# Kernel optimization log

Measured on AMD Instinct MI355X. Metric: run time of the kernel, lower is better.

The kernel has to match this reference:

```python
import jax, jax.numpy as jnp
import numpy as np

BETA = 0.25  # commitment loss weight (module default beta=0.25)
K = 1024     # num_of_embeddings


def setup_inputs() -> dict:
    key = jax.random.key(0)
    k1, k2 = jax.random.split(key)
    inputs = jax.random.normal(k1, (16, 256, 64, 64), dtype=jnp.float32)  # NCHW
    codebook = jax.random.normal(k2, (K, 256), dtype=jnp.float32)         # [K, D]
    return {"inputs": inputs, "codebook": codebook}


def reference(inputs, codebook):
    # NCHW -> NHWC, flatten to [N, D]
    x = jnp.transpose(inputs, (0, 2, 3, 1))
    shape_nhwc = x.shape
    flat = x.reshape(-1, codebook.shape[1])  # [N, D]

    dist = (jnp.sum(flat * flat, axis=1, keepdims=True)
            + jnp.sum(codebook * codebook, axis=1)
            - 2.0 * flat @ codebook.T)  # [N, K]
    idx = jnp.argmin(dist, axis=1)  # [N]

    # one-hot @ codebook is just a gather
    zq = codebook[idx].reshape(shape_nhwc)  # [B, H, W, D]

    commitment_loss = jnp.mean((zq - x) ** 2)
    loss = BETA * commitment_loss

    # straight-through estimator
    zq_st = x + jax.lax.stop_gradient(zq - x)

    # perplexity: avg one-hot probs == normalized histogram of code usage
    n = flat.shape[0]
    counts = jnp.zeros((K,), dtype=flat.dtype).at[idx].add(1.0)
    avg_probs = counts / n
    perplexity = jnp.exp(-jnp.sum(avg_probs * jnp.log(avg_probs + 1e-10)))

    z_out = jnp.transpose(zq_st, (0, 3, 1, 2))  # back to NCHW
    return z_out, loss, perplexity, idx[:, None]
```

## Files before the change

### kernel.cpp

```cpp
#include <hip/hip_runtime.h>
#include <math.h>

#define NPTS   65536
#define DDIM   256
#define KCODES 1024
#define HWSZ   4096
#define ZELEMS 16777216
#define CHW    1048576


typedef __attribute__((ext_vector_type(8))) short s16x8;
typedef __attribute__((ext_vector_type(4))) float f32x4;

#define AS1 __attribute__((address_space(1)))
#define AS3 __attribute__((address_space(3)))

__device__ __forceinline__ void bf16split(float x, unsigned short& h, unsigned short& l) {
    unsigned u  = __float_as_uint(x);
    unsigned hu = (u + 0x8000u) & 0xFFFF0000u;
    h = (unsigned short)(hu >> 16);
    float r = x - __uint_as_float(hu);
    l = (unsigned short)((__float_as_uint(r) + 0x8000u) >> 16);
}

__global__ __launch_bounds__(256) void conv_w(const float* __restrict__ cb,
                                              unsigned short* __restrict__ Ws,
                                              float* __restrict__ ww) {
    int gid  = blockIdx.x * 256 + threadIdx.x;
    int code = gid >> 3, o32 = gid & 7;
    int ct = code >> 8, r256 = code & 255, rh = r256 >> 7, rr = r256 & 127;
    unsigned short hi[32], lo[32];
    float ss = 0.f;
#pragma unroll
    for (int j4 = 0; j4 < 8; ++j4) {
        float4 v = *(const float4*)(cb + (size_t)code * DDIM + o32 * 32 + j4 * 4);
        ss += v.x * v.x + v.y * v.y + v.z * v.z + v.w * v.w;
        bf16split(v.x, hi[j4*4+0], lo[j4*4+0]);
        bf16split(v.y, hi[j4*4+1], lo[j4*4+1]);
        bf16split(v.z, hi[j4*4+2], lo[j4*4+2]);
        bf16split(v.w, hi[j4*4+3], lo[j4*4+3]);
    }
    ss += __shfl_down(ss, 4, 8);
    ss += __shfl_down(ss, 2, 8);
    ss += __shfl_down(ss, 1, 8);
    if (o32 == 0) ww[code] = ss;
    size_t bh = (size_t)ct * 131072 + (size_t)o32       * 8192 + rh * 4096 + (rr >> 4) * 512;
    size_t bl = (size_t)ct * 131072 + (size_t)(o32 + 8) * 8192 + rh * 4096 + (rr >> 4) * 512;
#pragma unroll
    for (int oct = 0; oct < 4; ++oct) {
        size_t fo = (size_t)((rr & 15) + 16 * oct) * 8;
        *(s16x8*)(Ws + bh + fo) = *(const s16x8*)&hi[oct * 8];
        *(s16x8*)(Ws + bl + fo) = *(const s16x8*)&lo[oct * 8];
    }
}

__global__ __launch_bounds__(256) void conv_x(const float* __restrict__ in,
                                              unsigned short* __restrict__ Xs,
                                              float* __restrict__ xxpart) {
    __shared__ float xt[32 * 128];
    __shared__ float xps[4];
    const int tid = threadIdx.x;
    const int rg = blockIdx.x >> 3, dc = blockIdx.x & 7;
    const int mt = rg >> 1, rhalf = rg & 1;
    const int b = (rg * 128) >> 12, hw0 = (rg * 128) & 4095;
    const float* src = in + (size_t)b * CHW + (size_t)(dc * 32) * HWSZ + hw0;
    float xs = 0.f;
#pragma unroll
    for (int r = 0; r < 16; ++r) {
        int e = r * 256 + tid, dd = e >> 7, i = e & 127;
        float v = src[(size_t)dd * HWSZ + i];
        xt[dd * 128 + i] = v;
        xs += v * v;
    }
#pragma unroll
    for (int o = 32; o; o >>= 1) xs += __shfl_down(xs, o, 64);
    if ((tid & 63) == 0) xps[tid >> 6] = xs;
    __syncthreads();
    if (tid == 0) xxpart[blockIdx.x] = xps[0] + xps[1] + xps[2] + xps[3];
#pragma unroll
    for (int hl = 0; hl < 2; ++hl) {
        int g = hl * 256 + tid;
        int row = g >> 2, o = g & 3;
        unsigned short hi[8], lo[8];
#pragma unroll
        for (int j = 0; j < 8; ++j)
            bf16split(xt[(o * 8 + j) * 128 + row], hi[j], lo[j]);
        size_t fo = rhalf * 4096 + (size_t)(row >> 4) * 512 + (size_t)((row & 15) + 16 * o) * 8;
        size_t bh = (size_t)mt * 131072 + (size_t)dc       * 8192 + fo;
        size_t bl = (size_t)mt * 131072 + (size_t)(dc + 8) * 8192 + fo;
        *(s16x8*)(Xs + bh) = *(const s16x8*)hi;
        *(s16x8*)(Xs + bl) = *(const s16x8*)lo;
    }
}

__global__ __launch_bounds__(512) void gemm_argmin(
        const unsigned short* __restrict__ Xs, const unsigned short* __restrict__ Ws,
        const float* __restrict__ ww, unsigned long long* __restrict__ pbest) {
    __shared__ unsigned short lds[49152];
    const int tid = threadIdx.x, lane = tid & 63, w = tid >> 6;
    const int wm = w >> 2, wn = w & 3;
    const int col = lane & 15, q = lane >> 4;
    const int bid = blockIdx.x;
    const int xcd = bid & 7, slot = bid >> 3;
    const int nt = slot & 3, mb = (slot >> 2) * 8 + xcd;

    const unsigned short* XsB = Xs + (size_t)mb * 131072;
    const unsigned short* WsB = Ws + (size_t)nt * 131072
                              + (wn >> 1) * 4096 + (wn & 1) * 2048 + lane * 8;

    f32x4 acc[8][4] = {};
    s16x8 B0[4], B1[4];
    const int aoff = wm * 4096 + lane * 8;

    auto SA = [&](int g, int p) {
        const int kA = (g & 7) | ((g >> 4) << 3);
        const unsigned short* s0 = XsB + kA * 8192 + tid * 8;
        __builtin_amdgcn_global_load_lds((const AS1 unsigned*)s0,
            (AS3 unsigned*)&lds[p * 8192 + w * 512], 16, 0, 0);
        __builtin_amdgcn_global_load_lds((const AS1 unsigned*)(s0 + 4096),
            (AS3 unsigned*)&lds[p * 8192 + 4096 + w * 512], 16, 0, 0);
    };
    auto LB = [&](int g, s16x8* B) {
        const int kW = (g & 7) | (((g >> 3) & 1) << 3);
        const s16x8* src = (const s16x8*)(WsB + kW * 8192);
        B[0] = src[0]; B[1] = src[64]; B[2] = src[128]; B[3] = src[192];
    };
#define BAR do { __builtin_amdgcn_s_barrier(); __builtin_amdgcn_sched_barrier(0); } while (0)

    auto TILE = [&](int g, int p, int pstg, const s16x8* Bc, s16x8* Bn,
                    int gate, bool dobar) {
        s16x8 a[8];
#pragma unroll
        for (int mf = 0; mf < 8; ++mf)
            a[mf] = *(const s16x8*)&lds[p * 8192 + aoff + mf * 512];
        if (g + 1 < 24) LB(g + 1, Bn);
        if (g + 4 < 24) SA(g + 4, pstg);
        if (gate == 6)      asm volatile("s_waitcnt vmcnt(6)" ::: "memory");
        else if (gate == 4) asm volatile("s_waitcnt vmcnt(4)" ::: "memory");
        else                asm volatile("s_waitcnt vmcnt(0)" ::: "memory");
        __builtin_amdgcn_sched_barrier(0);
        __builtin_amdgcn_s_setprio(1);
#pragma unroll
        for (int mf = 0; mf < 8; ++mf) {
            acc[mf][0] = __builtin_amdgcn_mfma_f32_16x16x32_bf16(a[mf], Bc[0], acc[mf][0], 0, 0, 0);
            acc[mf][1] = __builtin_amdgcn_mfma_f32_16x16x32_bf16(a[mf], Bc[1], acc[mf][1], 0, 0, 0);
            acc[mf][2] = __builtin_amdgcn_mfma_f32_16x16x32_bf16(a[mf], Bc[2], acc[mf][2], 0, 0, 0);
            acc[mf][3] = __builtin_amdgcn_mfma_f32_16x16x32_bf16(a[mf], Bc[3], acc[mf][3], 0, 0, 0);
        }
        __builtin_amdgcn_s_setprio(0);
        if (dobar) BAR;
    };

    SA(0, 0); SA(1, 1); SA(2, 2); SA(3, 3);
    LB(0, B0);
    asm volatile("s_waitcnt vmcnt(4)" ::: "memory");
    BAR;

    for (int t6 = 0; t6 < 3; ++t6) {
        TILE(t6 * 6 + 0, 0, 4, B0, B1, 6, false);
        TILE(t6 * 6 + 1, 1, 5, B1, B0, 6, true);
        TILE(t6 * 6 + 2, 2, 0, B0, B1, 6, false);
        TILE(t6 * 6 + 3, 3, 1, B1, B0, 6, true);
        TILE(t6 * 6 + 4, 4, 2, B0, B1, 6, false);
        TILE(t6 * 6 + 5, 5, 3, B1, B0, 6, true);
    }
    TILE(18, 0, 4, B0, B1, 6, false);
    TILE(19, 1, 5, B1, B0, 6, true);
    TILE(20, 2, 0, B0, B1, 4, false);
    TILE(21, 3, 1, B1, B0, 4, true);
    TILE(22, 4, 2, B0, B1, 4, false);
    TILE(23, 5, 3, B1, B0, 0, false);

    __syncthreads();
    unsigned long long* kbuf = (unsigned long long*)lds;
    float wv[4];
#pragma unroll
    for (int nf = 0; nf < 4; ++nf) wv[nf] = ww[nt * 256 + wn * 64 + nf * 16 + col];
#pragma unroll
    for (int mf = 0; mf < 8; ++mf)
#pragma unroll
        for (int r = 0; r < 4; ++r) {
            unsigned long long key = ~0ull;
#pragma unroll
            for (int nf = 0; nf < 4; ++nf) {
                int kg = nt * 256 + wn * 64 + nf * 16 + col;
                float sd = wv[nf] - 2.f * acc[mf][nf][r];
                unsigned u = __float_as_uint(sd);
                u = (u & 0x80000000u) ? ~u : (u | 0x80000000u);
                unsigned long long kk = ((unsigned long long)u << 32) | (unsigned)kg;
                key = kk < key ? kk : key;
            }
#pragma unroll
            for (int off = 1; off < 4; off <<= 1) {
                unsigned klo = __shfl_xor((unsigned)key, off, 64);
                unsigned khi = __shfl_xor((unsigned)(key >> 32), off, 64);
                unsigned long long ok = ((unsigned long long)khi << 32) | klo;
                key = ok < key ? ok : key;
            }
            if ((col & 3) == 0)
                kbuf[(wm * 128 + mf * 16 + q * 4 + r) * 17 + wn * 4 + (col >> 2)] = key;
        }
    __syncthreads();
    if (tid < 256) {
        const unsigned long long* rowp = kbuf + tid * 17;
        unsigned long long km = rowp[0];
#pragma unroll
        for (int i = 1; i < 16; ++i) {
            unsigned long long k = rowp[i];
            km = k < km ? k : km;
        }
        pbest[(size_t)nt * 65536 + mb * 256 + tid] = km;
    }
#undef BAR
}

__global__ __launch_bounds__(256) void gather_kernel(
        const float* __restrict__ cb, const unsigned long long* __restrict__ pbest,
        float* __restrict__ idx_out, unsigned int* __restrict__ counts,
        float* __restrict__ zout, float* __restrict__ partials) {
    const int tid = threadIdx.x;
    const int n   = blockIdx.x * 256 + tid;
    unsigned long long km = pbest[n];
#pragma unroll
    for (int nt = 1; nt < 4; ++nt) {
        unsigned long long k = pbest[(size_t)nt * 65536 + n];
        km = k < km ? k : km;
    }
    const int r = (int)(km & 0xFFFFFFFFu);
    idx_out[n] = (float)r;
    atomicAdd(&counts[r], 1u);

    unsigned m = (unsigned)(km >> 32);
    m = (m & 0x80000000u) ? (m & 0x7FFFFFFFu) : ~m;
    float sd = __uint_as_float(m);

    const int b = n >> 12, hw = n & 4095;
    const float4* row4 = (const float4*)(cb + (size_t)r * DDIM);
    float* zp = zout + (size_t)b * CHW + hw;
#pragma unroll 8
    for (int c4 = 0; c4 < 64; ++c4) {
        float4 v = row4[c4];
        zp[(size_t)(c4 * 4 + 0) * HWSZ] = v.x;
        zp[(size_t)(c4 * 4 + 1) * HWSZ] = v.y;
        zp[(size_t)(c4 * 4 + 2) * HWSZ] = v.z;
        zp[(size_t)(c4 * 4 + 3) * HWSZ] = v.w;
    }
#pragma unroll
    for (int o = 32; o; o >>= 1) sd += __shfl_down(sd, o, 64);
    __shared__ float ps[4];
    if ((tid & 63) == 0) ps[tid >> 6] = sd;
    __syncthreads();
    if (tid == 0) partials[blockIdx.x] = ps[0] + ps[1] + ps[2] + ps[3];
}

__global__ __launch_bounds__(256) void final_kernel(
        const float* __restrict__ partials, const float* __restrict__ xxpart,
        const unsigned int* __restrict__ counts,
        float* __restrict__ out_loss, float* __restrict__ out_perp) {
    const int tid = threadIdx.x;
    float s = partials[tid];
#pragma unroll
    for (int i = 0; i < 16; ++i) s += xxpart[tid * 16 + i];
    float e = 0.f;
#pragma unroll
    for (int qq = 0; qq < 4; ++qq) {
        float p = (float)counts[tid * 4 + qq] * (1.f / 65536.f);
        e += p * logf(p + 1e-10f);
    }
#pragma unroll
    for (int o = 32; o; o >>= 1) {
        s += __shfl_down(s, o, 64);
        e += __shfl_down(e, o, 64);
    }
    __shared__ float ss[4], es[4];
    if ((tid & 63) == 0) { ss[tid >> 6] = s; es[tid >> 6] = e; }
    __syncthreads();
    if (tid == 0) {
        float S = ss[0] + ss[1] + ss[2] + ss[3];
        float E = es[0] + es[1] + es[2] + es[3];
        *out_loss = 0.25f * (S / (float)ZELEMS);
        *out_perp = expf(-E);
    }
}

extern "C" void kernel_launch(void* const* d_in, const int* in_sizes, int n_in,
                              void* d_out, int out_size, void* d_ws, size_t ws_size,
                              hipStream_t stream) {
    (void)in_sizes; (void)n_in; (void)out_size; (void)ws_size;
    const float* in = (const float*)d_in[0];
    const float* cb = (const float*)d_in[1];
    float* out  = (float*)d_out;
    float* zout = out;
    float* loss = out + ZELEMS;
    float* perp = out + ZELEMS + 1;
    float* idxf = out + ZELEMS + 2;

    unsigned int*       counts   = (unsigned int*)d_ws;
    float*              ww       = (float*)((char*)d_ws + 4096);
    float*              partials = (float*)((char*)d_ws + 8192);
    unsigned short*     Ws       = (unsigned short*)((char*)d_ws + 16384);
    unsigned long long* pbest    = (unsigned long long*)((char*)d_ws + 1064960);
    float*              xxpart   = (float*)((char*)d_ws + 3162112);
    unsigned short*     Xs       = (unsigned short*)zout;

    hipMemsetAsync(counts, 0, 4096, stream);
    conv_w      <<<32,   256, 0, stream>>>(cb, Ws, ww);
    conv_x      <<<4096, 256, 0, stream>>>(in, Xs, xxpart);
    gemm_argmin <<<1024, 512, 0, stream>>>(Xs, Ws, ww, pbest);
    gather_kernel<<<256, 256, 0, stream>>>(cb, pbest, idxf, counts, zout, partials);
    final_kernel <<<1,   256, 0, stream>>>(partials, xxpart, counts, loss, perp);
}
```

Measured before the change: 188.7 us.

## Load GEMM A fragments directly from global into registers, dropping LDS staging

The GEMM-argmin kernel no longer stages X tiles through shared memory with global_load_lds and a 4-deep ring of barriers and vmcnt gates. Each wave now loads its A and B fragments straight from global memory into registers, double-buffered two steps ahead. This removes barriers and LDS traffic. In exchange, A data that was shared across the four wn waves is now fetched redundantly from global/L2, register pressure rises, and latency hiding depends on the compiler's scheduling.

Result: slower. 529.7 us (+180.7%).

```diff
diff --git a/kernel.cpp b/kernel.cpp
--- a/kernel.cpp
+++ b/kernel.cpp
@@ -11,9 +11,6 @@
 
 typedef __attribute__((ext_vector_type(8))) short s16x8;
 typedef __attribute__((ext_vector_type(4))) float f32x4;
-
-#define AS1 __attribute__((address_space(1)))
-#define AS3 __attribute__((address_space(3)))
 
 __device__ __forceinline__ void bf16split(float x, unsigned short& h, unsigned short& l) {
     unsigned u  = __float_as_uint(x);
@@ -96,7 +93,7 @@
 __global__ __launch_bounds__(512) void gemm_argmin(
         const unsigned short* __restrict__ Xs, const unsigned short* __restrict__ Ws,
         const float* __restrict__ ww, unsigned long long* __restrict__ pbest) {
-    __shared__ unsigned short lds[49152];
+    __shared__ unsigned long long kbuf[256 * 17];
     const int tid = threadIdx.x, lane = tid & 63, w = tid >> 6;
     const int wm = w >> 2, wn = w & 3;
     const int col = lane & 15, q = lane >> 4;
@@ -104,75 +101,44 @@
     const int xcd = bid & 7, slot = bid >> 3;
     const int nt = slot & 3, mb = (slot >> 2) * 8 + xcd;
 
-    const unsigned short* XsB = Xs + (size_t)mb * 131072;
-    const unsigned short* WsB = Ws + (size_t)nt * 131072
-                              + (wn >> 1) * 4096 + (wn & 1) * 2048 + lane * 8;
+    const unsigned short* Aw = Xs + (size_t)mb * 131072 + wm * 4096 + lane * 8;
+    const unsigned short* Bw = Ws + (size_t)nt * 131072
+                             + (wn >> 1) * 4096 + (wn & 1) * 2048 + lane * 8;
 
     f32x4 acc[8][4] = {};
-    s16x8 B0[4], B1[4];
-    const int aoff = wm * 4096 + lane * 8;
-
-    auto SA = [&](int g, int p) {
+    s16x8 A0[8], A1[8], B0[4], B1[4];
+
+    auto LA = [&](int g, s16x8* A) {
         const int kA = (g & 7) | ((g >> 4) << 3);
-        const unsigned short* s0 = XsB + kA * 8192 + tid * 8;
-        __builtin_amdgcn_global_load_lds((const AS1 unsigned*)s0,
-            (AS3 unsigned*)&lds[p * 8192 + w * 512], 16, 0, 0);
-        __builtin_amdgcn_global_load_lds((const AS1 unsigned*)(s0 + 4096),
-            (AS3 unsigned*)&lds[p * 8192 + 4096 + w * 512], 16, 0, 0);
+        const unsigned short* src = Aw + kA * 8192;
+#pragma unroll
+        for (int mf = 0; mf < 8; ++mf) A[mf] = *(const s16x8*)(src + mf * 512);
     };
     auto LB = [&](int g, s16x8* B) {
         const int kW = (g & 7) | (((g >> 3) & 1) << 3);
-        const s16x8* src = (const s16x8*)(WsB + kW * 8192);
-        B[0] = src[0]; B[1] = src[64]; B[2] = src[128]; B[3] = src[192];
+        const unsigned short* src = Bw + kW * 8192;
+#pragma unroll
+        for (int nf = 0; nf < 4; ++nf) B[nf] = *(const s16x8*)(src + nf * 512);
     };
-#define BAR do { __builtin_amdgcn_s_barrier(); __builtin_amdgcn_sched_barrier(0); } while (0)
-
-    auto TILE = [&](int g, int p, int pstg, const s16x8* Bc, s16x8* Bn,
-                    int gate, bool dobar) {
-        s16x8 a[8];
-#pragma unroll
-        for (int mf = 0; mf < 8; ++mf)
-            a[mf] = *(const s16x8*)&lds[p * 8192 + aoff + mf * 512];
-        if (g + 1 < 24) LB(g + 1, Bn);
-        if (g + 4 < 24) SA(g + 4, pstg);
-        if (gate == 6)      asm volatile("s_waitcnt vmcnt(6)" ::: "memory");
-        else if (gate == 4) asm volatile("s_waitcnt vmcnt(4)" ::: "memory");
-        else                asm volatile("s_waitcnt vmcnt(0)" ::: "memory");
-        __builtin_amdgcn_sched_barrier(0);
-        __builtin_amdgcn_s_setprio(1);
+    auto STEP = [&](int g, s16x8* Ac, s16x8* Bc) {
 #pragma unroll
         for (int mf = 0; mf < 8; ++mf) {
-            acc[mf][0] = __builtin_amdgcn_mfma_f32_16x16x32_bf16(a[mf], Bc[0], acc[mf][0], 0, 0, 0);
-            acc[mf][1] = __builtin_amdgcn_mfma_f32_16x16x32_bf16(a[mf], Bc[1], acc[mf][1], 0, 0, 0);
-            acc[mf][2] = __builtin_amdgcn_mfma_f32_16x16x32_bf16(a[mf], Bc[2], acc[mf][2], 0, 0, 0);
-            acc[mf][3] = __builtin_amdgcn_mfma_f32_16x16x32_bf16(a[mf], Bc[3], acc[mf][3], 0, 0, 0);
+            acc[mf][0] = __builtin_amdgcn_mfma_f32_16x16x32_bf16(Ac[mf], Bc[0], acc[mf][0], 0, 0, 0);
+            acc[mf][1] = __builtin_amdgcn_mfma_f32_16x16x32_bf16(Ac[mf], Bc[1], acc[mf][1], 0, 0, 0);
+            acc[mf][2] = __builtin_amdgcn_mfma_f32_16x16x32_bf16(Ac[mf], Bc[2], acc[mf][2], 0, 0, 0);
+            acc[mf][3] = __builtin_amdgcn_mfma_f32_16x16x32_bf16(Ac[mf], Bc[3], acc[mf][3], 0, 0, 0);
         }
-        __builtin_amdgcn_s_setprio(0);
-        if (dobar) BAR;
+        if (g + 2 < 24) { LA(g + 2, Ac); LB(g + 2, Bc); }
     };
 
-    SA(0, 0); SA(1, 1); SA(2, 2); SA(3, 3);
-    LB(0, B0);
-    asm volatile("s_waitcnt vmcnt(4)" ::: "memory");
-    BAR;
-
-    for (int t6 = 0; t6 < 3; ++t6) {
-        TILE(t6 * 6 + 0, 0, 4, B0, B1, 6, false);
-        TILE(t6 * 6 + 1, 1, 5, B1, B0, 6, true);
-        TILE(t6 * 6 + 2, 2, 0, B0, B1, 6, false);
-        TILE(t6 * 6 + 3, 3, 1, B1, B0, 6, true);
-        TILE(t6 * 6 + 4, 4, 2, B0, B1, 6, false);
-        TILE(t6 * 6 + 5, 5, 3, B1, B0, 6, true);
-    }
-    TILE(18, 0, 4, B0, B1, 6, false);
-    TILE(19, 1, 5, B1, B0, 6, true);
-    TILE(20, 2, 0, B0, B1, 4, false);
-    TILE(21, 3, 1, B1, B0, 4, true);
-    TILE(22, 4, 2, B0, B1, 4, false);
-    TILE(23, 5, 3, B1, B0, 0, false);
-
-    __syncthreads();
-    unsigned long long* kbuf = (unsigned long long*)lds;
+    LA(0, A0); LB(0, B0);
+    LA(1, A1); LB(1, B1);
+#pragma unroll
+    for (int gg = 0; gg < 12; ++gg) {
+        STEP(2 * gg,     A0, B0);
+        STEP(2 * gg + 1, A1, B1);
+    }
+
     float wv[4];
 #pragma unroll
     for (int nf = 0; nf < 4; ++nf) wv[nf] = ww[nt * 256 + wn * 64 + nf * 16 + col];
@@ -211,7 +177,6 @@
         }
         pbest[(size_t)nt * 65536 + mb * 256 + tid] = km;
     }
-#undef BAR
 }
 
 __global__ __launch_bounds__(256) void gather_kernel(
```

## Halve GEMM M-tile to 128 rows, double grid, raise occupancy

Applied to the files above, without the earlier changes.

The fused distance-GEMM/argmin kernel now covers 128 rows per block instead of 256. Accumulators shrink to 4x4, LDS drops to 48 KB, and the grid doubles to 2048 blocks with launch_bounds(512,4). The vmcnt wait also moves from before the MFMAs to just before the barrier. The aim is more resident waves to hide latency, at the cost of loading the W fragments from global twice as often per output row. The looser wait placement may race with the LDS staging.

After: 179.4 us. 4.9% less time.

```diff
diff --git a/kernel.cpp b/kernel.cpp
--- a/kernel.cpp
+++ b/kernel.cpp
@@ -93,62 +93,59 @@
     }
 }
 
-__global__ __launch_bounds__(512) void gemm_argmin(
+__global__ __launch_bounds__(512, 4) void gemm_argmin(
         const unsigned short* __restrict__ Xs, const unsigned short* __restrict__ Ws,
         const float* __restrict__ ww, unsigned long long* __restrict__ pbest) {
-    __shared__ unsigned short lds[49152];
+    __shared__ unsigned short lds[24576];
     const int tid = threadIdx.x, lane = tid & 63, w = tid >> 6;
     const int wm = w >> 2, wn = w & 3;
     const int col = lane & 15, q = lane >> 4;
     const int bid = blockIdx.x;
     const int xcd = bid & 7, slot = bid >> 3;
-    const int nt = slot & 3, mb = (slot >> 2) * 8 + xcd;
-
-    const unsigned short* XsB = Xs + (size_t)mb * 131072;
-    const unsigned short* WsB = Ws + (size_t)nt * 131072
+    const int nt = slot & 3, mbi = (slot >> 2) * 8 + xcd;
+    const int mt = mbi >> 1, rh = mbi & 1;
+
+    const unsigned short* XsB = Xs + (size_t)mt * 131072 + rh * 4096;
+    const unsigned short* Bw  = Ws + (size_t)nt * 131072
                               + (wn >> 1) * 4096 + (wn & 1) * 2048 + lane * 8;
 
-    f32x4 acc[8][4] = {};
+    f32x4 acc[4][4] = {};
     s16x8 B0[4], B1[4];
-    const int aoff = wm * 4096 + lane * 8;
+    const int aoff = wm * 2048 + lane * 8;
 
     auto SA = [&](int g, int p) {
         const int kA = (g & 7) | ((g >> 4) << 3);
-        const unsigned short* s0 = XsB + kA * 8192 + tid * 8;
-        __builtin_amdgcn_global_load_lds((const AS1 unsigned*)s0,
-            (AS3 unsigned*)&lds[p * 8192 + w * 512], 16, 0, 0);
-        __builtin_amdgcn_global_load_lds((const AS1 unsigned*)(s0 + 4096),
-            (AS3 unsigned*)&lds[p * 8192 + 4096 + w * 512], 16, 0, 0);
+        __builtin_amdgcn_global_load_lds(
+            (const AS1 unsigned*)(XsB + kA * 8192 + tid * 8),
+            (AS3 unsigned*)&lds[p * 4096 + (tid >> 6) * 512 + (tid & 63) * 8], 16, 0, 0);
     };
     auto LB = [&](int g, s16x8* B) {
         const int kW = (g & 7) | (((g >> 3) & 1) << 3);
-        const s16x8* src = (const s16x8*)(WsB + kW * 8192);
+        const s16x8* src = (const s16x8*)(Bw + kW * 8192);
         B[0] = src[0]; B[1] = src[64]; B[2] = src[128]; B[3] = src[192];
     };
 #define BAR do { __builtin_amdgcn_s_barrier(); __builtin_amdgcn_sched_barrier(0); } while (0)
 
-    auto TILE = [&](int g, int p, int pstg, const s16x8* Bc, s16x8* Bn,
-                    int gate, bool dobar) {
-        s16x8 a[8];
-#pragma unroll
-        for (int mf = 0; mf < 8; ++mf)
-            a[mf] = *(const s16x8*)&lds[p * 8192 + aoff + mf * 512];
+    auto TILE = [&](int g, int p, int pstg, const s16x8* Bc, s16x8* Bn, bool sync) {
+        s16x8 a[4];
+#pragma unroll
+        for (int mf = 0; mf < 4; ++mf)
+            a[mf] = *(const s16x8*)&lds[p * 4096 + aoff + mf * 512];
         if (g + 1 < 24) LB(g + 1, Bn);
         if (g + 4 < 24) SA(g + 4, pstg);
-        if (gate == 6)      asm volatile("s_waitcnt vmcnt(6)" ::: "memory");
-        else if (gate == 4) asm volatile("s_waitcnt vmcnt(4)" ::: "memory");
-        else                asm volatile("s_waitcnt vmcnt(0)" ::: "memory");
-        __builtin_amdgcn_sched_barrier(0);
         __builtin_amdgcn_s_setprio(1);
 #pragma unroll
-        for (int mf = 0; mf < 8; ++mf) {
+        for (int mf = 0; mf < 4; ++mf) {
             acc[mf][0] = __builtin_amdgcn_mfma_f32_16x16x32_bf16(a[mf], Bc[0], acc[mf][0], 0, 0, 0);
             acc[mf][1] = __builtin_amdgcn_mfma_f32_16x16x32_bf16(a[mf], Bc[1], acc[mf][1], 0, 0, 0);
             acc[mf][2] = __builtin_amdgcn_mfma_f32_16x16x32_bf16(a[mf], Bc[2], acc[mf][2], 0, 0, 0);
             acc[mf][3] = __builtin_amdgcn_mfma_f32_16x16x32_bf16(a[mf], Bc[3], acc[mf][3], 0, 0, 0);
         }
         __builtin_amdgcn_s_setprio(0);
-        if (dobar) BAR;
+        if (sync) {
+            asm volatile("s_waitcnt vmcnt(5)" ::: "memory");
+            BAR;
+        }
     };
 
     SA(0, 0); SA(1, 1); SA(2, 2); SA(3, 3);
@@ -157,19 +154,19 @@
     BAR;
 
     for (int t6 = 0; t6 < 3; ++t6) {
-        TILE(t6 * 6 + 0, 0, 4, B0, B1, 6, false);
-        TILE(t6 * 6 + 1, 1, 5, B1, B0, 6, true);
-        TILE(t6 * 6 + 2, 2, 0, B0, B1, 6, false);
-        TILE(t6 * 6 + 3, 3, 1, B1, B0, 6, true);
-        TILE(t6 * 6 + 4, 4, 2, B0, B1, 6, false);
-        TILE(t6 * 6 + 5, 5, 3, B1, B0, 6, true);
-    }
-    TILE(18, 0, 4, B0, B1, 6, false);
-    TILE(19, 1, 5, B1, B0, 6, true);
-    TILE(20, 2, 0, B0, B1, 4, false);
-    TILE(21, 3, 1, B1, B0, 4, true);
-    TILE(22, 4, 2, B0, B1, 4, false);
-    TILE(23, 5, 3, B1, B0, 0, false);
+        TILE(t6 * 6 + 0, 0, 4, B0, B1, false);
+        TILE(t6 * 6 + 1, 1, 5, B1, B0, true);
+        TILE(t6 * 6 + 2, 2, 0, B0, B1, false);
+        TILE(t6 * 6 + 3, 3, 1, B1, B0, true);
+        TILE(t6 * 6 + 4, 4, 2, B0, B1, false);
+        TILE(t6 * 6 + 5, 5, 3, B1, B0, true);
+    }
+    TILE(18, 0, 4, B0, B1, false);
+    TILE(19, 1, 5, B1, B0, true);
+    TILE(20, 2, 0, B0, B1, false);
+    TILE(21, 3, 1, B1, B0, true);
+    TILE(22, 4, 2, B0, B1, false);
+    TILE(23, 5, 3, B1, B0, false);
 
     __syncthreads();
     unsigned long long* kbuf = (unsigned long long*)lds;
@@ -177,7 +174,7 @@
 #pragma unroll
     for (int nf = 0; nf < 4; ++nf) wv[nf] = ww[nt * 256 + wn * 64 + nf * 16 + col];
 #pragma unroll
-    for (int mf = 0; mf < 8; ++mf)
+    for (int mf = 0; mf < 4; ++mf)
 #pragma unroll
         for (int r = 0; r < 4; ++r) {
             unsigned long long key = ~0ull;
@@ -198,10 +195,10 @@
                 key = ok < key ? ok : key;
             }
             if ((col & 3) == 0)
-                kbuf[(wm * 128 + mf * 16 + q * 4 + r) * 17 + wn * 4 + (col >> 2)] = key;
+                kbuf[(wm * 64 + mf * 16 + q * 4 + r) * 17 + wn * 4 + (col >> 2)] = key;
         }
     __syncthreads();
-    if (tid < 256) {
+    if (tid < 128) {
         const unsigned long long* rowp = kbuf + tid * 17;
         unsigned long long km = rowp[0];
 #pragma unroll
@@ -209,7 +206,7 @@
             unsigned long long k = rowp[i];
             km = k < km ? k : km;
         }
-        pbest[(size_t)nt * 65536 + mb * 256 + tid] = km;
+        pbest[(size_t)nt * 65536 + mbi * 128 + tid] = km;
     }
 #undef BAR
 }
@@ -306,7 +303,7 @@
     hipMemsetAsync(counts, 0, 4096, stream);
     conv_w      <<<32,   256, 0, stream>>>(cb, Ws, ww);
     conv_x      <<<4096, 256, 0, stream>>>(in, Xs, xxpart);
-    gemm_argmin <<<1024, 512, 0, stream>>>(Xs, Ws, ww, pbest);
+    gemm_argmin <<<2048, 512, 0, stream>>>(Xs, Ws, ww, pbest);
     gather_kernel<<<256, 256, 0, stream>>>(cb, pbest, idxf, counts, zout, partials);
     final_kernel <<<1,   256, 0, stream>>>(partials, xxpart, counts, loss, perp);
 }
```
